# Optimization experiments

Measured on AMD Instinct MI355X. Metric: run time of the kernel, lower is better.

## Reference

```python
import jax, jax.numpy as jnp
import numpy as np

H = 16
D = 1024
DK = D // H


def setup_inputs() -> dict:
    key = jax.random.key(0)
    ks = jax.random.split(key, 10)
    B, S = 2, 2048
    scale = 1.0 / np.sqrt(D)
    inp = {
        "query": jax.random.normal(ks[0], (B, S, D), jnp.float32),
        "key_": jax.random.normal(ks[1], (B, S, D), jnp.float32),
        "value": jax.random.normal(ks[2], (B, S, D), jnp.float32),
        "Wq": jax.random.normal(ks[3], (D, D), jnp.float32) * scale,
        "bq": jnp.zeros((D,), jnp.float32),
        "Wk": jax.random.normal(ks[4], (D, D), jnp.float32) * scale,
        "bk": jnp.zeros((D,), jnp.float32),
        "Wv": jax.random.normal(ks[5], (D, D), jnp.float32) * scale,
        "bv": jnp.zeros((D,), jnp.float32),
        "ln_gamma": jnp.ones((D,), jnp.float32),
        "ln_beta": jnp.zeros((D,), jnp.float32),
    }
    return inp


def reference(query, key_, value, Wq, bq, Wk, bk, Wv, bv, ln_gamma, ln_beta):
    B, S, _ = query.shape
    residual = query
    # projections, split into heads: [B, H, S, DK]
    def proj(x, W, b):
        return (x @ W + b).reshape(B, -1, H, DK).transpose(0, 2, 1, 3)
    q = proj(query, Wq, bq)
    k = proj(key_, Wk, bk)
    v = proj(value, Wv, bv)
    # scaled dot-product attention with full score matrix (as in source)
    scores = jnp.einsum("bhqd,bhkd->bhqk", q, k) / jnp.sqrt(jnp.float32(DK))
    p_att = jax.nn.softmax(scores, axis=-1)  # dropout p=0 -> identity
    x = jnp.einsum("bhqk,bhkd->bhqd", p_att, v)
    x = x.transpose(0, 2, 1, 3).reshape(B, S, D)
    # residual + LayerNorm(eps=1e-6)
    y = x + residual
    mu = jnp.mean(y, axis=-1, keepdims=True)
    var = jnp.var(y, axis=-1, keepdims=True)
    y = (y - mu) / jnp.sqrt(var + 1e-6)
    return y * ln_gamma + ln_beta
```

## Files before the change

kernel.cpp:

```cpp
#include <hip/hip_runtime.h>


typedef float f32x4 __attribute__((ext_vector_type(4)));
typedef short short8 __attribute__((ext_vector_type(8)));
typedef unsigned int uint32x4 __attribute__((ext_vector_type(4)));

__device__ __forceinline__ unsigned short f2bf(float f) {
    unsigned u = __builtin_bit_cast(unsigned, f);
    u += 0x7fffu + ((u >> 16) & 1u);
    return (unsigned short)(u >> 16);
}
__device__ __forceinline__ unsigned packbf2(float lo, float hi) {
    return __builtin_amdgcn_perm(__builtin_bit_cast(unsigned, hi),
                                 __builtin_bit_cast(unsigned, lo), 0x07060302u);
}

__device__ __forceinline__ void g2l16(const unsigned short* g, unsigned short* l) {
    __builtin_amdgcn_global_load_lds(
        (const __attribute__((address_space(1))) unsigned int*)g,
        (__attribute__((address_space(3))) unsigned int*)l, 16, 0, 0);
}

__global__ __launch_bounds__(256) void convert_all(
    const float* __restrict__ xq, const float* __restrict__ xk, const float* __restrict__ xv,
    const float* __restrict__ Wq, const float* __restrict__ Wk, const float* __restrict__ Wv,
    unsigned short* __restrict__ xout, unsigned short* __restrict__ wout)
{
    const int bx  = blockIdx.x;
    const int tid = threadIdx.x;
    if (bx < 6144) {
        const int z = bx >> 11;
        const float* src = (z == 0) ? xq : (z == 1) ? xk : xv;
        const size_t idx = ((size_t)(bx & 2047) * 256 + tid) * 8;
        const float4 a = *(const float4*)(src + idx);
        const float4 b = *(const float4*)(src + idx + 4);
        short8 o;
        o[0] = (short)f2bf(a.x); o[1] = (short)f2bf(a.y);
        o[2] = (short)f2bf(a.z); o[3] = (short)f2bf(a.w);
        o[4] = (short)f2bf(b.x); o[5] = (short)f2bf(b.y);
        o[6] = (short)f2bf(b.z); o[7] = (short)f2bf(b.w);
        *(short8*)(xout + (size_t)z * 4194304 + idx) = o;
    } else {
        const int i = bx - 6144;
        const int z = i >> 8, tile = i & 255;
        const float* W = (z == 0) ? Wq : (z == 1) ? Wk : Wv;
        unsigned short* Wt = wout + (size_t)z * 1048576;
        __shared__ unsigned short Ts[64 * 65];
        const int kb0 = (tile >> 4) * 64, nb0 = (tile & 15) * 64;
        const int a = tid >> 6, b = tid & 63;
#pragma unroll
        for (int j = 0; j < 16; ++j) {
            const int k = j * 4 + a, n = b;
            Ts[n * 65 + k] = f2bf(W[(size_t)(kb0 + k) * 1024 + nb0 + n]);
        }
        __syncthreads();
#pragma unroll
        for (int j = 0; j < 16; ++j) {
            const int n = j * 4 + a, k = b;
            Wt[(size_t)(nb0 + n) * 1024 + kb0 + k] = Ts[n * 65 + k];
        }
    }
}

__global__ __launch_bounds__(256) void qkv_gemm(
    const unsigned short* __restrict__ Xb, const unsigned short* __restrict__ Wtb,
    const float* __restrict__ bq, const float* __restrict__ bk, const float* __restrict__ bv,
    unsigned short* __restrict__ qo, unsigned short* __restrict__ ko, unsigned short* __restrict__ vo)
{
    const int z = blockIdx.z;
    const unsigned short* X  = Xb  + (size_t)z * 4194304;
    const unsigned short* Wt = Wtb + (size_t)z * 1048576;
    const float* bias   = (z == 0) ? bq : (z == 1) ? bk : bv;
    unsigned short* out = (z == 0) ? qo : (z == 1) ? ko : vo;

    __shared__ unsigned short smem[16384];

    const int tid  = threadIdx.x;
    const int wave = tid >> 6;
    const int lane = tid & 63;
    const int l15  = lane & 15;
    const int quad = lane >> 4;
    const int mq   = wave & 1, nq = wave >> 1;
    const int mbase = blockIdx.x * 128, nbase = blockIdx.y * 128;

    const int srow = lane >> 2;
    const int schk = (lane & 3) ^ (srow & 3);

    const unsigned short* srcA = X  + (size_t)(mbase + wave * 32 + srow) * 1024 + schk * 8;
    const unsigned short* srcB = Wt + (size_t)(nbase + wave * 32 + srow) * 1024 + schk * 8;

    f32x4 acc[4][4];
#pragma unroll
    for (int i = 0; i < 4; ++i)
#pragma unroll
        for (int j = 0; j < 4; ++j) acc[i][j] = (f32x4){0.f, 0.f, 0.f, 0.f};

#pragma unroll
    for (int t = 0; t < 2; ++t) {
        g2l16(srcA + (size_t)t * 16 * 1024, &smem[(wave * 32 + t * 16) * 32]);
        g2l16(srcB + (size_t)t * 16 * 1024, &smem[4096 + (wave * 32 + t * 16) * 32]);
    }

    for (int it = 0; it < 32; ++it) {
        const int boff = (it & 1) * 8192;
        __syncthreads();

        if (it + 1 < 32) {
            const int poff = boff ^ 8192;
            const size_t ko2 = (size_t)(it + 1) * 32;
#pragma unroll
            for (int t = 0; t < 2; ++t) {
                g2l16(srcA + (size_t)t * 16 * 1024 + ko2, &smem[poff + (wave * 32 + t * 16) * 32]);
                g2l16(srcB + (size_t)t * 16 * 1024 + ko2, &smem[poff + 4096 + (wave * 32 + t * 16) * 32]);
            }
        }

        short8 af[4], bf[4];
#pragma unroll
        for (int i = 0; i < 4; ++i) {
            af[i] = *(const short8*)(&smem[boff + (mq * 64 + i * 16 + l15) * 32 + ((quad ^ (l15 & 3)) << 3)]);
            bf[i] = *(const short8*)(&smem[boff + 4096 + (nq * 64 + i * 16 + l15) * 32 + ((quad ^ (l15 & 3)) << 3)]);
        }
#pragma unroll
        for (int mt = 0; mt < 4; ++mt)
#pragma unroll
            for (int nt = 0; nt < 4; ++nt)
                acc[mt][nt] = __builtin_amdgcn_mfma_f32_16x16x32_bf16(af[mt], bf[nt], acc[mt][nt], 0, 0, 0);
    }

    __syncthreads();

    float bvals[4];
#pragma unroll
    for (int nt = 0; nt < 4; ++nt) bvals[nt] = bias[nbase + nq * 64 + nt * 16 + l15];

    if (z == 2) {
        unsigned short* Epv = smem;
        const int hbase = nbase >> 6;
        const int b     = mbase >> 11;
        const int srow0 = mbase & 2047;
#pragma unroll
        for (int nt = 0; nt < 4; ++nt) {
            __syncthreads();
            short8 w[2];
#pragma unroll
            for (int e = 0; e < 2; ++e)
#pragma unroll
                for (int j = 0; j < 8; ++j) {
                    const int mt2 = 2 * e + (j >> 2), r = j & 3;
                    w[e][j] = (short)f2bf(acc[mt2][nt][r] + bvals[nt]);
                }
            unsigned short* dst = &Epv[(nq * 16 + l15) * 136 + mq * 64 + quad * 8];
            *(short8*)(dst)      = w[0];
            *(short8*)(dst + 32) = w[1];
            __syncthreads();
            const int row = tid >> 3;
            const int d   = nt * 16 + (row & 15);
            const int h   = hbase + (row >> 4);
#pragma unroll
            for (int e = 0; e < 2; ++e) {
                const int colb = e * 64 + (tid & 7) * 8;
                short8 v = *(const short8*)(&Epv[row * 136 + colb]);
                *(short8*)(&out[((size_t)(b * 16 + h) * 64 + d) * 2048 + srow0 + colb]) = v;
            }
        }
    } else {
        unsigned short* Ep = smem + wave * 1152;
        const int hQ = (nbase + nq * 64) >> 6;
        const float scl = (z == 0) ? 0.18033688f : 1.0f;
#pragma unroll
        for (int mt = 0; mt < 4; ++mt) {
#pragma unroll
            for (int nt = 0; nt < 4; ++nt)
#pragma unroll
                for (int r = 0; r < 4; ++r)
                    Ep[(quad * 4 + r) * 72 + nt * 16 + l15] =
                        f2bf((acc[mt][nt][r] + bvals[nt]) * scl);
#pragma unroll
            for (int half = 0; half < 2; ++half) {
                const int m = (lane >> 3) + half * 8;
                const int nblk = lane & 7;
                short8 v = *(const short8*)(&Ep[m * 72 + nblk * 8]);
                const int gm = mbase + mq * 64 + mt * 16 + m;
                const int b2 = gm >> 11, srw = gm & 2047;
                *(short8*)(&out[((size_t)(b2 * 16 + hQ) * 2048 + srw) * 64 + nblk * 8]) = v;
            }
        }
    }
}

__global__ __launch_bounds__(256) void attn(
    const unsigned short* __restrict__ qb, const unsigned short* __restrict__ kb,
    const unsigned short* __restrict__ vtb, float* __restrict__ xw)
{
    const int tid  = threadIdx.x;
    const int wave = tid >> 6;
    const int lane = tid & 63;
    const int l15  = lane & 15;
    const int quad = lane >> 4;

    const int bh    = blockIdx.x;
    const int qbase = blockIdx.y * 128 + wave * 32;

    __shared__ unsigned short Ks[2][64 * 64];
    __shared__ unsigned short Vs[2][64 * 64];
    __shared__ float Ow[4][32 * 68];

    short8 qf[2][2];
#pragma unroll
    for (int nt = 0; nt < 2; ++nt) {
        const unsigned short* Qp = qb + ((size_t)bh * 2048 + qbase + nt * 16 + l15) * 64 + quad * 8;
        qf[nt][0] = *(const short8*)(Qp);
        qf[nt][1] = *(const short8*)(Qp + 32);
    }

    const unsigned short* Kbh = kb  + (size_t)bh * 2048 * 64;
    const unsigned short* Vbh = vtb + (size_t)bh * 64 * 2048;

    const int r8 = lane >> 3, c8 = lane & 7;
    const unsigned short *srcK[2], *srcV[2];
#pragma unroll
    for (int t = 0; t < 2; ++t) {
        const int row = wave * 16 + t * 8 + r8;
        srcK[t] = Kbh + (size_t)row * 64   + ((c8 ^ r8) << 3);
        srcV[t] = Vbh + (size_t)row * 2048 + ((c8 ^ r8) << 3);
    }

    float l_part[2] = {0.f, 0.f};
    f32x4 O[2][4];
#pragma unroll
    for (int nt = 0; nt < 2; ++nt)
#pragma unroll
        for (int i = 0; i < 4; ++i) O[nt][i] = (f32x4){0.f, 0.f, 0.f, 0.f};

#pragma unroll
    for (int t = 0; t < 2; ++t) {
        g2l16(srcK[t], &Ks[0][(wave * 16 + t * 8) * 64]);
        g2l16(srcV[t], &Vs[0][(wave * 16 + t * 8) * 64]);
    }

    for (int it = 0; it < 32; ++it) {
        const int buf = it & 1;
        __syncthreads();

        if (it + 1 < 32) {
            const size_t kn = (size_t)(it + 1) * 64;
#pragma unroll
            for (int t = 0; t < 2; ++t) {
                g2l16(srcK[t] + kn * 64, &Ks[buf ^ 1][(wave * 16 + t * 8) * 64]);
                g2l16(srcV[t] + kn,      &Vs[buf ^ 1][(wave * 16 + t * 8) * 64]);
            }
        }

        short8 kf[4][2];
#pragma unroll
        for (int mt = 0; mt < 4; ++mt)
#pragma unroll
            for (int dc = 0; dc < 2; ++dc)
                kf[mt][dc] = *(const short8*)(&Ks[buf][(mt * 16 + l15) * 64 +
                                                  ((((dc << 2) + quad) ^ (l15 & 7)) << 3)]);

        f32x4 sc[4][2];
#pragma unroll
        for (int mt = 0; mt < 4; ++mt)
#pragma unroll
            for (int nt = 0; nt < 2; ++nt) {
                f32x4 a = {0.f, 0.f, 0.f, 0.f};
                a = __builtin_amdgcn_mfma_f32_16x16x32_bf16(kf[mt][0], qf[nt][0], a, 0, 0, 0);
                a = __builtin_amdgcn_mfma_f32_16x16x32_bf16(kf[mt][1], qf[nt][1], a, 0, 0, 0);
                sc[mt][nt] = a;
            }

#pragma unroll
        for (int mt = 0; mt < 4; ++mt)
#pragma unroll
            for (int nt = 0; nt < 2; ++nt) {
#pragma unroll
                for (int r = 0; r < 4; ++r) {
                    const float p = __builtin_amdgcn_exp2f(sc[mt][nt][r]);
                    sc[mt][nt][r] = p;
                    l_part[nt] += p;
                }
            }

#pragma unroll
        for (int c = 0; c < 2; ++c) {
            short8 pf[2];
#pragma unroll
            for (int nt = 0; nt < 2; ++nt) {
                uint32x4 pu;
                pu[0] = packbf2(sc[2 * c][nt][0],     sc[2 * c][nt][1]);
                pu[1] = packbf2(sc[2 * c][nt][2],     sc[2 * c][nt][3]);
                pu[2] = packbf2(sc[2 * c + 1][nt][0], sc[2 * c + 1][nt][1]);
                pu[3] = packbf2(sc[2 * c + 1][nt][2], sc[2 * c + 1][nt][3]);
                pf[nt] = __builtin_bit_cast(short8, pu);
            }
#pragma unroll
            for (int dt = 0; dt < 4; ++dt) {
                const short8 vf = *(const short8*)(&Vs[buf][(dt * 16 + l15) * 64 +
                                                       ((((c << 2) + quad) ^ (l15 & 7)) << 3)]);
                O[0][dt] = __builtin_amdgcn_mfma_f32_16x16x32_bf16(vf, pf[0], O[0][dt], 0, 0, 0);
                O[1][dt] = __builtin_amdgcn_mfma_f32_16x16x32_bf16(vf, pf[1], O[1][dt], 0, 0, 0);
            }
        }
    }

    float inv[2];
#pragma unroll
    for (int nt = 0; nt < 2; ++nt) {
        float s = l_part[nt];
        s += __shfl_xor(s, 16);
        s += __shfl_xor(s, 32);
        inv[nt] = 1.0f / s;
    }

#pragma unroll
    for (int nt = 0; nt < 2; ++nt)
#pragma unroll
        for (int dt = 0; dt < 4; ++dt) {
            f32x4 v = O[nt][dt];
            v[0] *= inv[nt]; v[1] *= inv[nt]; v[2] *= inv[nt]; v[3] *= inv[nt];
            *(f32x4*)(&Ow[wave][(nt * 16 + l15) * 68 + dt * 16 + quad * 4]) = v;
        }

    const int b = bh >> 4, h = bh & 15;
    const size_t obase = ((size_t)b * 2048 + qbase) * 1024 + h * 64 + lane;
#pragma unroll
    for (int qq = 0; qq < 32; ++qq)
        xw[obase + (size_t)qq * 1024] = Ow[wave][qq * 68 + lane];
}

__global__ __launch_bounds__(256) void ln_kernel(
    const float* __restrict__ xw, const float* __restrict__ res,
    const float* __restrict__ gamma, const float* __restrict__ beta,
    float* __restrict__ out)
{
    const int row = blockIdx.x;
    const int tid = threadIdx.x;
    const size_t base = (size_t)row * 1024 + tid * 4;

    const float4 x  = *(const float4*)(xw + base);
    const float4 rv = *(const float4*)(res + base);
    float4 y;
    y.x = x.x + rv.x; y.y = x.y + rv.y; y.z = x.z + rv.z; y.w = x.w + rv.w;

    float s  = y.x + y.y + y.z + y.w;
    float s2 = y.x * y.x + y.y * y.y + y.z * y.z + y.w * y.w;
#pragma unroll
    for (int off = 32; off >= 1; off >>= 1) {
        s  += __shfl_xor(s, off);
        s2 += __shfl_xor(s2, off);
    }
    __shared__ float red[8];
    const int wave = tid >> 6;
    if ((tid & 63) == 0) { red[wave] = s; red[4 + wave] = s2; }
    __syncthreads();
    s  = red[0] + red[1] + red[2] + red[3];
    s2 = red[4] + red[5] + red[6] + red[7];

    const float mu   = s * (1.0f / 1024.0f);
    const float var  = s2 * (1.0f / 1024.0f) - mu * mu;
    const float rstd = rsqrtf(var + 1e-6f);

    const float4 g  = *(const float4*)(gamma + tid * 4);
    const float4 bt = *(const float4*)(beta + tid * 4);
    float4 o;
    o.x = (y.x - mu) * rstd * g.x + bt.x;
    o.y = (y.y - mu) * rstd * g.y + bt.y;
    o.z = (y.z - mu) * rstd * g.z + bt.z;
    o.w = (y.w - mu) * rstd * g.w + bt.w;
    *(float4*)(out + base) = o;
}

extern "C" void kernel_launch(void* const* d_in, const int* in_sizes, int n_in,
                              void* d_out, int out_size, void* d_ws, size_t ws_size,
                              hipStream_t stream) {
    const float* query = (const float*)d_in[0];
    const float* key_  = (const float*)d_in[1];
    const float* value = (const float*)d_in[2];
    const float* Wq    = (const float*)d_in[3];
    const float* bq    = (const float*)d_in[4];
    const float* Wk    = (const float*)d_in[5];
    const float* bk    = (const float*)d_in[6];
    const float* Wv    = (const float*)d_in[7];
    const float* bv    = (const float*)d_in[8];
    const float* ln_g  = (const float*)d_in[9];
    const float* ln_b  = (const float*)d_in[10];
    float* out = (float*)d_out;

    const size_t MB = 1024 * 1024;
    char* ws = (char*)d_ws;
    unsigned short* Xbuf = (unsigned short*)(ws);
    float*          xwp  = (float*)(ws);
    unsigned short* Wtb  = (unsigned short*)(ws + 24 * MB);
    unsigned short* qbuf = (unsigned short*)(ws + 30 * MB);
    unsigned short* kbuf = (unsigned short*)(ws + 38 * MB);
    unsigned short* vtb  = (unsigned short*)(ws + 46 * MB);

    convert_all<<<6912,           256, 0, stream>>>(query, key_, value, Wq, Wk, Wv, Xbuf, Wtb);
    qkv_gemm   <<<dim3(32, 8, 3), 256, 0, stream>>>(Xbuf, Wtb, bq, bk, bv, qbuf, kbuf, vtb);
    attn       <<<dim3(32, 16),   256, 0, stream>>>(qbuf, kbuf, vtb, xwp);
    ln_kernel  <<<4096,           256, 0, stream>>>(xwp, query, ln_g, ln_b, out);
}
```

Measured before the change: 205.6 us.

## Split attention KV range across two wave groups and compute row sums with MFMA

The attention kernel now launches 512 threads per block, and two groups of four waves each process half of the key/value sequence for the same query tile. Partial outputs are combined through swizzled shared memory at the end, and the two halves' softmax denominators are summed there. The per-element softmax denominator accumulation is replaced by an MFMA against a ones vector, which removes scalar adds and cross-lane shuffles. This roughly halves the serial loop length per block and raises waves per CU, at the cost of extra shared-memory reduction, more barriers, and row sums taken from bf16-rounded probabilities.

```diff
diff --git a/kernel.cpp b/kernel.cpp
--- a/kernel.cpp
+++ b/kernel.cpp
@@ -189,22 +189,26 @@
     }
 }
 
-__global__ __launch_bounds__(256) void attn(
+__global__ __launch_bounds__(512, 4) void attn(
     const unsigned short* __restrict__ qb, const unsigned short* __restrict__ kb,
     const unsigned short* __restrict__ vtb, float* __restrict__ xw)
 {
     const int tid  = threadIdx.x;
     const int wave = tid >> 6;
+    const int wq   = wave & 3;
+    const int kvh  = wave >> 2;
     const int lane = tid & 63;
     const int l15  = lane & 15;
     const int quad = lane >> 4;
 
     const int bh    = blockIdx.x;
-    const int qbase = blockIdx.y * 128 + wave * 32;
-
-    __shared__ unsigned short Ks[2][64 * 64];
-    __shared__ unsigned short Vs[2][64 * 64];
-    __shared__ float Ow[4][32 * 68];
+    const int qbase = blockIdx.y * 128 + wq * 32;
+
+    __shared__ __align__(16) unsigned short smem[32768];
+    __shared__ float Lsh[8][32];
+
+    unsigned short* Ks0 = smem + kvh * 16384;
+    unsigned short* Vs0 = Ks0 + 8192;
 
     short8 qf[2][2];
 #pragma unroll
@@ -214,50 +218,58 @@
         qf[nt][1] = *(const short8*)(Qp + 32);
     }
 
-    const unsigned short* Kbh = kb  + (size_t)bh * 2048 * 64;
-    const unsigned short* Vbh = vtb + (size_t)bh * 64 * 2048;
+    const unsigned short* Kbh = kb  + ((size_t)bh * 2048 + (size_t)kvh * 1024) * 64;
+    const unsigned short* Vbh = vtb + (size_t)bh * 64 * 2048 + (size_t)kvh * 1024;
 
     const int r8 = lane >> 3, c8 = lane & 7;
     const unsigned short *srcK[2], *srcV[2];
 #pragma unroll
     for (int t = 0; t < 2; ++t) {
-        const int row = wave * 16 + t * 8 + r8;
+        const int row = wq * 16 + t * 8 + r8;
         srcK[t] = Kbh + (size_t)row * 64   + ((c8 ^ r8) << 3);
         srcV[t] = Vbh + (size_t)row * 2048 + ((c8 ^ r8) << 3);
     }
 
-    float l_part[2] = {0.f, 0.f};
+    uint32x4 ou; ou[0] = ou[1] = ou[2] = ou[3] = 0x3F803F80u;
+    const short8 onesf = __builtin_bit_cast(short8, ou);
+
+    f32x4 lacc[2];
     f32x4 O[2][4];
 #pragma unroll
-    for (int nt = 0; nt < 2; ++nt)
+    for (int nt = 0; nt < 2; ++nt) {
+        lacc[nt] = (f32x4){0.f, 0.f, 0.f, 0.f};
 #pragma unroll
         for (int i = 0; i < 4; ++i) O[nt][i] = (f32x4){0.f, 0.f, 0.f, 0.f};
+    }
 
 #pragma unroll
     for (int t = 0; t < 2; ++t) {
-        g2l16(srcK[t], &Ks[0][(wave * 16 + t * 8) * 64]);
-        g2l16(srcV[t], &Vs[0][(wave * 16 + t * 8) * 64]);
-    }
-
-    for (int it = 0; it < 32; ++it) {
+        g2l16(srcK[t], Ks0 + (wq * 16 + t * 8) * 64);
+        g2l16(srcV[t], Vs0 + (wq * 16 + t * 8) * 64);
+    }
+
+    for (int it = 0; it < 16; ++it) {
         const int buf = it & 1;
         __syncthreads();
 
-        if (it + 1 < 32) {
+        if (it + 1 < 16) {
             const size_t kn = (size_t)(it + 1) * 64;
 #pragma unroll
             for (int t = 0; t < 2; ++t) {
-                g2l16(srcK[t] + kn * 64, &Ks[buf ^ 1][(wave * 16 + t * 8) * 64]);
-                g2l16(srcV[t] + kn,      &Vs[buf ^ 1][(wave * 16 + t * 8) * 64]);
-            }
-        }
+                g2l16(srcK[t] + kn * 64, Ks0 + (buf ^ 1) * 4096 + (wq * 16 + t * 8) * 64);
+                g2l16(srcV[t] + kn,      Vs0 + (buf ^ 1) * 4096 + (wq * 16 + t * 8) * 64);
+            }
+        }
+
+        const unsigned short* Kb_ = Ks0 + buf * 4096;
+        const unsigned short* Vb_ = Vs0 + buf * 4096;
 
         short8 kf[4][2];
 #pragma unroll
         for (int mt = 0; mt < 4; ++mt)
 #pragma unroll
             for (int dc = 0; dc < 2; ++dc)
-                kf[mt][dc] = *(const short8*)(&Ks[buf][(mt * 16 + l15) * 64 +
+                kf[mt][dc] = *(const short8*)(&Kb_[(mt * 16 + l15) * 64 +
                                                   ((((dc << 2) + quad) ^ (l15 & 7)) << 3)]);
 
         f32x4 sc[4][2];
@@ -274,14 +286,10 @@
 #pragma unroll
         for (int mt = 0; mt < 4; ++mt)
 #pragma unroll
-            for (int nt = 0; nt < 2; ++nt) {
-#pragma unroll
-                for (int r = 0; r < 4; ++r) {
-                    const float p = __builtin_amdgcn_exp2f(sc[mt][nt][r]);
-                    sc[mt][nt][r] = p;
-                    l_part[nt] += p;
-                }
-            }
+            for (int nt = 0; nt < 2; ++nt)
+#pragma unroll
+                for (int r = 0; r < 4; ++r)
+                    sc[mt][nt][r] = __builtin_amdgcn_exp2f(sc[mt][nt][r]);
 
 #pragma unroll
         for (int c = 0; c < 2; ++c) {
@@ -295,9 +303,11 @@
                 pu[3] = packbf2(sc[2 * c + 1][nt][2], sc[2 * c + 1][nt][3]);
                 pf[nt] = __builtin_bit_cast(short8, pu);
             }
+            lacc[0] = __builtin_amdgcn_mfma_f32_16x16x32_bf16(onesf, pf[0], lacc[0], 0, 0, 0);
+            lacc[1] = __builtin_amdgcn_mfma_f32_16x16x32_bf16(onesf, pf[1], lacc[1], 0, 0, 0);
 #pragma unroll
             for (int dt = 0; dt < 4; ++dt) {
-                const short8 vf = *(const short8*)(&Vs[buf][(dt * 16 + l15) * 64 +
+                const short8 vf = *(const short8*)(&Vb_[(dt * 16 + l15) * 64 +
                                                        ((((c << 2) + quad) ^ (l15 & 7)) << 3)]);
                 O[0][dt] = __builtin_amdgcn_mfma_f32_16x16x32_bf16(vf, pf[0], O[0][dt], 0, 0, 0);
                 O[1][dt] = __builtin_amdgcn_mfma_f32_16x16x32_bf16(vf, pf[1], O[1][dt], 0, 0, 0);
@@ -305,29 +315,35 @@
         }
     }
 
-    float inv[2];
-#pragma unroll
-    for (int nt = 0; nt < 2; ++nt) {
-        float s = l_part[nt];
-        s += __shfl_xor(s, 16);
-        s += __shfl_xor(s, 32);
-        inv[nt] = 1.0f / s;
-    }
-
+    __syncthreads();
+
+    if (quad == 0) {
+        Lsh[wave][l15]      = lacc[0][0];
+        Lsh[wave][16 + l15] = lacc[1][0];
+    }
+
+    float* Ow = (float*)smem + wave * 2048;
 #pragma unroll
     for (int nt = 0; nt < 2; ++nt)
 #pragma unroll
         for (int dt = 0; dt < 4; ++dt) {
-            f32x4 v = O[nt][dt];
-            v[0] *= inv[nt]; v[1] *= inv[nt]; v[2] *= inv[nt]; v[3] *= inv[nt];
-            *(f32x4*)(&Ow[wave][(nt * 16 + l15) * 68 + dt * 16 + quad * 4]) = v;
-        }
-
+            const int row  = nt * 16 + l15;
+            const int c4s  = (dt * 4 + quad) ^ l15;
+            *(f32x4*)(&Ow[row * 64 + c4s * 4]) = O[nt][dt];
+        }
+    __syncthreads();
+
+    const float* OwA = (float*)smem + wq * 2048;
+    const float* OwB = (float*)smem + (wq + 4) * 2048;
     const int b = bh >> 4, h = bh & 15;
     const size_t obase = ((size_t)b * 2048 + qbase) * 1024 + h * 64 + lane;
 #pragma unroll
-    for (int qq = 0; qq < 32; ++qq)
-        xw[obase + (size_t)qq * 1024] = Ow[wave][qq * 68 + lane];
+    for (int j = 0; j < 16; ++j) {
+        const int qq   = kvh * 16 + j;
+        const float li = 1.0f / (Lsh[wq][qq] + Lsh[wq + 4][qq]);
+        const int off  = qq * 64 + (((lane >> 2) ^ (qq & 15)) << 2) + (lane & 3);
+        xw[obase + (size_t)qq * 1024] = (OwA[off] + OwB[off]) * li;
+    }
 }
 
 __global__ __launch_bounds__(256) void ln_kernel(
@@ -399,6 +415,6 @@
 
     convert_all<<<6912,           256, 0, stream>>>(query, key_, value, Wq, Wk, Wv, Xbuf, Wtb);
     qkv_gemm   <<<dim3(32, 8, 3), 256, 0, stream>>>(Xbuf, Wtb, bq, bk, bv, qbuf, kbuf, vtb);
-    attn       <<<dim3(32, 16),   256, 0, stream>>>(qbuf, kbuf, vtb, xwp);
+    attn       <<<dim3(32, 16),   512, 0, stream>>>(qbuf, kbuf, vtb, xwp);
     ln_kernel  <<<4096,           256, 0, stream>>>(xwp, query, ln_g, ln_b, out);
 }
```

New measurement: 201.8 us. Within noise of the previous version (-1.9%).

## Load K/V fragments directly from global into registers, drop LDS staging

Applied to the files above, without the earlier changes.

The attention kernel no longer stages K and V tiles through double-buffered shared memory with barriers. Each wave now loads its MFMA fragments straight from global memory into registers, software-pipelined by alternating two K register sets. The softmax row sum is computed by an MFMA against a ones vector instead of scalar adds and shuffles, and the output staging buffer uses an XOR swizzle instead of padding. This removes the per-iteration __syncthreads and LDS traffic, but every wave now fetches the K/V tiles separately, with a less coalesced pattern, relying on the cache.

```diff
diff --git a/kernel.cpp b/kernel.cpp
--- a/kernel.cpp
+++ b/kernel.cpp
@@ -202,9 +202,7 @@
     const int bh    = blockIdx.x;
     const int qbase = blockIdx.y * 128 + wave * 32;
 
-    __shared__ unsigned short Ks[2][64 * 64];
-    __shared__ unsigned short Vs[2][64 * 64];
-    __shared__ float Ow[4][32 * 68];
+    __shared__ __align__(16) float Ow[4][2048];
 
     short8 qf[2][2];
 #pragma unroll
@@ -214,52 +212,40 @@
         qf[nt][1] = *(const short8*)(Qp + 32);
     }
 
-    const unsigned short* Kbh = kb  + (size_t)bh * 2048 * 64;
-    const unsigned short* Vbh = vtb + (size_t)bh * 64 * 2048;
-
-    const int r8 = lane >> 3, c8 = lane & 7;
-    const unsigned short *srcK[2], *srcV[2];
-#pragma unroll
-    for (int t = 0; t < 2; ++t) {
-        const int row = wave * 16 + t * 8 + r8;
-        srcK[t] = Kbh + (size_t)row * 64   + ((c8 ^ r8) << 3);
-        srcV[t] = Vbh + (size_t)row * 2048 + ((c8 ^ r8) << 3);
-    }
-
-    float l_part[2] = {0.f, 0.f};
+    const unsigned short* Kl = kb  + (size_t)bh * 2048 * 64 + (size_t)l15 * 64   + quad * 8;
+    const unsigned short* Vl = vtb + (size_t)bh * 64 * 2048 + (size_t)l15 * 2048 + quad * 8;
+
+    uint32x4 ou; ou[0] = ou[1] = ou[2] = ou[3] = 0x3F803F80u;
+    const short8 onesf = __builtin_bit_cast(short8, ou);
+
+    f32x4 lacc[2];
     f32x4 O[2][4];
 #pragma unroll
-    for (int nt = 0; nt < 2; ++nt)
+    for (int nt = 0; nt < 2; ++nt) {
+        lacc[nt] = (f32x4){0.f, 0.f, 0.f, 0.f};
 #pragma unroll
         for (int i = 0; i < 4; ++i) O[nt][i] = (f32x4){0.f, 0.f, 0.f, 0.f};
-
-#pragma unroll
-    for (int t = 0; t < 2; ++t) {
-        g2l16(srcK[t], &Ks[0][(wave * 16 + t * 8) * 64]);
-        g2l16(srcV[t], &Vs[0][(wave * 16 + t * 8) * 64]);
-    }
-
-    for (int it = 0; it < 32; ++it) {
-        const int buf = it & 1;
-        __syncthreads();
-
-        if (it + 1 < 32) {
-            const size_t kn = (size_t)(it + 1) * 64;
-#pragma unroll
-            for (int t = 0; t < 2; ++t) {
-                g2l16(srcK[t] + kn * 64, &Ks[buf ^ 1][(wave * 16 + t * 8) * 64]);
-                g2l16(srcV[t] + kn,      &Vs[buf ^ 1][(wave * 16 + t * 8) * 64]);
-            }
-        }
-
-        short8 kf[4][2];
-#pragma unroll
-        for (int mt = 0; mt < 4; ++mt)
-#pragma unroll
-            for (int dc = 0; dc < 2; ++dc)
-                kf[mt][dc] = *(const short8*)(&Ks[buf][(mt * 16 + l15) * 64 +
-                                                  ((((dc << 2) + quad) ^ (l15 & 7)) << 3)]);
-
+    }
+
+    short8 kfa[4][2], kfb[4][2], vf[4][2];
+
+    auto loadK = [&](short8 (&kf)[4][2], int it) {
+        const unsigned short* p = Kl + it * 4096;
+#pragma unroll
+        for (int mt = 0; mt < 4; ++mt) {
+            kf[mt][0] = *(const short8*)(p + mt * 1024);
+            kf[mt][1] = *(const short8*)(p + mt * 1024 + 32);
+        }
+    };
+    auto loadV = [&](int it) {
+        const unsigned short* p = Vl + it * 64;
+#pragma unroll
+        for (int dt = 0; dt < 4; ++dt) {
+            vf[dt][0] = *(const short8*)(p + dt * 32768);
+            vf[dt][1] = *(const short8*)(p + dt * 32768 + 32);
+        }
+    };
+    auto compute = [&](const short8 (&kf)[4][2]) {
         f32x4 sc[4][2];
 #pragma unroll
         for (int mt = 0; mt < 4; ++mt)
@@ -270,19 +256,13 @@
                 a = __builtin_amdgcn_mfma_f32_16x16x32_bf16(kf[mt][1], qf[nt][1], a, 0, 0, 0);
                 sc[mt][nt] = a;
             }
-
 #pragma unroll
         for (int mt = 0; mt < 4; ++mt)
 #pragma unroll
-            for (int nt = 0; nt < 2; ++nt) {
-#pragma unroll
-                for (int r = 0; r < 4; ++r) {
-                    const float p = __builtin_amdgcn_exp2f(sc[mt][nt][r]);
-                    sc[mt][nt][r] = p;
-                    l_part[nt] += p;
-                }
-            }
-
+            for (int nt = 0; nt < 2; ++nt)
+#pragma unroll
+                for (int r = 0; r < 4; ++r)
+                    sc[mt][nt][r] = __builtin_amdgcn_exp2f(sc[mt][nt][r]);
 #pragma unroll
         for (int c = 0; c < 2; ++c) {
             short8 pf[2];
@@ -295,39 +275,48 @@
                 pu[3] = packbf2(sc[2 * c + 1][nt][2], sc[2 * c + 1][nt][3]);
                 pf[nt] = __builtin_bit_cast(short8, pu);
             }
+            lacc[0] = __builtin_amdgcn_mfma_f32_16x16x32_bf16(onesf, pf[0], lacc[0], 0, 0, 0);
+            lacc[1] = __builtin_amdgcn_mfma_f32_16x16x32_bf16(onesf, pf[1], lacc[1], 0, 0, 0);
 #pragma unroll
             for (int dt = 0; dt < 4; ++dt) {
-                const short8 vf = *(const short8*)(&Vs[buf][(dt * 16 + l15) * 64 +
-                                                       ((((c << 2) + quad) ^ (l15 & 7)) << 3)]);
-                O[0][dt] = __builtin_amdgcn_mfma_f32_16x16x32_bf16(vf, pf[0], O[0][dt], 0, 0, 0);
-                O[1][dt] = __builtin_amdgcn_mfma_f32_16x16x32_bf16(vf, pf[1], O[1][dt], 0, 0, 0);
-            }
-        }
-    }
-
-    float inv[2];
+                O[0][dt] = __builtin_amdgcn_mfma_f32_16x16x32_bf16(vf[dt][c], pf[0], O[0][dt], 0, 0, 0);
+                O[1][dt] = __builtin_amdgcn_mfma_f32_16x16x32_bf16(vf[dt][c], pf[1], O[1][dt], 0, 0, 0);
+            }
+        }
+    };
+
+    loadK(kfa, 0);
+#pragma unroll 1
+    for (int it = 0; it < 32; it += 2) {
+        loadK(kfb, it + 1);
+        loadV(it);
+        compute(kfa);
+        if (it + 2 < 32) loadK(kfa, it + 2);
+        loadV(it + 1);
+        compute(kfb);
+    }
+
+    const float inv0 = 1.0f / lacc[0][0];
+    const float inv1 = 1.0f / lacc[1][0];
+    float* Owp = &Ow[wave][0];
 #pragma unroll
     for (int nt = 0; nt < 2; ++nt) {
-        float s = l_part[nt];
-        s += __shfl_xor(s, 16);
-        s += __shfl_xor(s, 32);
-        inv[nt] = 1.0f / s;
-    }
-
-#pragma unroll
-    for (int nt = 0; nt < 2; ++nt)
+        const float iv = nt ? inv1 : inv0;
 #pragma unroll
         for (int dt = 0; dt < 4; ++dt) {
             f32x4 v = O[nt][dt];
-            v[0] *= inv[nt]; v[1] *= inv[nt]; v[2] *= inv[nt]; v[3] *= inv[nt];
-            *(f32x4*)(&Ow[wave][(nt * 16 + l15) * 68 + dt * 16 + quad * 4]) = v;
-        }
-
+            v[0] *= iv; v[1] *= iv; v[2] *= iv; v[3] *= iv;
+            const int row = nt * 16 + l15;
+            const int c4s = (dt * 4 + quad) ^ l15;
+            *(f32x4*)(&Owp[row * 64 + c4s * 4]) = v;
+        }
+    }
     const int b = bh >> 4, h = bh & 15;
     const size_t obase = ((size_t)b * 2048 + qbase) * 1024 + h * 64 + lane;
 #pragma unroll
     for (int qq = 0; qq < 32; ++qq)
-        xw[obase + (size_t)qq * 1024] = Ow[wave][qq * 68 + lane];
+        xw[obase + (size_t)qq * 1024] =
+            Owp[qq * 64 + ((((lane >> 2) ^ (qq & 15)) << 2) | (lane & 3))];
 }
 
 __global__ __launch_bounds__(256) void ln_kernel(
```

New measurement: 276.6 us. 1.35x slower.
